# Kernel tuning notes

Hardware: AMD Instinct MI355X
Metric: run time of the kernel (lower is better)

## Reference

```python
import jax, jax.numpy as jnp
import numpy as np

D_MODEL = 1024
N_HEADS = 16
HIDDEN = int(D_MODEL * 4 * 2 / 3)  # 2730, matches torch int(d*4*2/3)
EPS = 1e-6


def setup_inputs() -> dict:
    key = jax.random.key(0)
    ks = jax.random.split(key, 8)
    B, T = 4, 2048
    s = 0.02
    return {
        "x": jax.random.normal(ks[0], (B, T, D_MODEL), dtype=jnp.float32),
        "w_attn": jax.random.normal(ks[1], (D_MODEL, 3 * D_MODEL), dtype=jnp.float32) * s,
        "w_proj": jax.random.normal(ks[2], (D_MODEL, D_MODEL), dtype=jnp.float32) * s,
        "w1": jax.random.normal(ks[3], (D_MODEL, HIDDEN), dtype=jnp.float32) * s,
        "w2": jax.random.normal(ks[4], (D_MODEL, HIDDEN), dtype=jnp.float32) * s,
        "w3": jax.random.normal(ks[5], (HIDDEN, D_MODEL), dtype=jnp.float32) * s,
        "g1": jnp.ones((D_MODEL,), dtype=jnp.float32),
        "g2": jnp.ones((D_MODEL,), dtype=jnp.float32),
    }


def rmsnorm(x, g):
    norm = jax.lax.rsqrt(jnp.mean(x * x, axis=-1, keepdims=True) + EPS)
    return x * norm * g


def reference(x, w_attn, w_proj, w1, w2, w3, g1, g2):
    B, T, C = x.shape
    H = N_HEADS
    hd = C // H

    # attention branch
    qkv = rmsnorm(x, g1) @ w_attn                     # [B,T,3C]
    q, k, v = jnp.split(qkv, 3, axis=-1)
    q = q.reshape(B, T, H, hd).transpose(0, 2, 1, 3)  # [B,H,T,hd]
    k = k.reshape(B, T, H, hd).transpose(0, 2, 1, 3)
    v = v.reshape(B, T, H, hd).transpose(0, 2, 1, 3)

    att = jnp.einsum("bhqd,bhkd->bhqk", q, k) / jnp.sqrt(jnp.float32(hd))
    causal = jnp.tril(jnp.ones((T, T), dtype=bool))
    att = jnp.where(causal[None, None], att, jnp.float32(-jnp.inf))
    att = jax.nn.softmax(att, axis=-1)
    y = jnp.einsum("bhqk,bhkd->bhqd", att, v)          # [B,H,T,hd]
    y = y.transpose(0, 2, 1, 3).reshape(B, T, C)
    attn_out = y @ w_proj

    # parallel MLP branch on ln_2(x) (note: applied to x, not x+attn)
    h = rmsnorm(x, g2)
    mlp_out = (jax.nn.silu(h @ w1) * (h @ w2)) @ w3

    # dropout is identity in eval mode
    return x + attn_out + mlp_out
```

## Files before the change

### kernel.cpp

```cpp
#include <hip/hip_runtime.h>

#define TT 2048
#define DM 1024
#define HPAD 2816
#define HID 2730

typedef __attribute__((ext_vector_type(4))) float f32x4;
typedef __attribute__((ext_vector_type(8))) short bf16x8;

static __device__ __forceinline__ float bf2f(short u) {
    union { float f; unsigned int i; } c; c.i = ((unsigned int)(unsigned short)u) << 16; return c.f;
}
static __device__ __forceinline__ short f2bf(float f) {
    union { float f; unsigned int i; } c; c.f = f;
    unsigned int i = c.i;
    unsigned int r = (i + 0x7fffu + ((i >> 16) & 1u)) >> 16;
    return (short)r;
}
static __device__ __forceinline__ unsigned int fbits(float f) {
    union { float f; unsigned int i; } c; c.f = f;
    return c.i;
}

static __device__ __forceinline__ void gload_lds16(const void* g, void* l) {
    __builtin_amdgcn_global_load_lds(
        (const __attribute__((address_space(1))) unsigned int*)g,
        (__attribute__((address_space(3))) unsigned int*)l, 16, 0, 0);
}

__global__ __launch_bounds__(256) void wprep(const float* __restrict__ in, short* __restrict__ out,
                                             int K, int N, int Kpad, int Npad) {
    __shared__ float tile[32][33];
    int kb = blockIdx.x * 32, nb = blockIdx.y * 32;
    int tx = threadIdx.x, ty = threadIdx.y;
    #pragma unroll
    for (int i = 0; i < 32; i += 8) {
        int k = kb + ty + i, n = nb + tx;
        float v = (k < K && n < N) ? in[(size_t)k * N + n] : 0.f;
        tile[tx][ty + i] = v;
    }
    __syncthreads();
    #pragma unroll
    for (int i = 0; i < 32; i += 8) {
        int n = nb + ty + i, k = kb + tx;
        if (n < Npad && k < Kpad) out[(size_t)n * Kpad + k] = f2bf(tile[ty + i][tx]);
    }
}

__global__ __launch_bounds__(256) void rmsnorm2(const float* __restrict__ x,
    const float* __restrict__ g1, const float* __restrict__ g2,
    short* __restrict__ xn1, short* __restrict__ xn2) {
    int row = blockIdx.x;
    const float* xr = x + (size_t)row * DM;
    int t = threadIdx.x;
    float4 v = ((const float4*)xr)[t];
    float ss = v.x*v.x + v.y*v.y + v.z*v.z + v.w*v.w;
    #pragma unroll
    for (int off = 1; off < 64; off <<= 1) ss += __shfl_xor(ss, off);
    __shared__ float red[4];
    if ((t & 63) == 0) red[t >> 6] = ss;
    __syncthreads();
    float tot = red[0] + red[1] + red[2] + red[3];
    float rs = rsqrtf(tot * (1.0f / DM) + 1e-6f);
    float4 G1 = ((const float4*)g1)[t];
    float4 G2 = ((const float4*)g2)[t];
    union { short s[4]; int2 v; } o1, o2;
    o1.s[0] = f2bf(v.x * rs * G1.x); o1.s[1] = f2bf(v.y * rs * G1.y);
    o1.s[2] = f2bf(v.z * rs * G1.z); o1.s[3] = f2bf(v.w * rs * G1.w);
    o2.s[0] = f2bf(v.x * rs * G2.x); o2.s[1] = f2bf(v.y * rs * G2.y);
    o2.s[2] = f2bf(v.z * rs * G2.z); o2.s[3] = f2bf(v.w * rs * G2.w);
    *(int2*)(xn1 + (size_t)row * DM + t * 4) = o1.v;
    *(int2*)(xn2 + (size_t)row * DM + t * 4) = o2.v;
}

template<int EPI>
__global__ __launch_bounds__(256) void gemm_bt(
    const short* __restrict__ A, const short* __restrict__ Bt,
    short* __restrict__ Cb, const float* __restrict__ X, float* __restrict__ Of,
    int M, int N, int K)
{
    __shared__ short As[128 * 64];
    __shared__ short Bs[128 * 64];
    int t = threadIdx.x;
    int wid = t >> 6, l = t & 63;
    int wm = wid >> 1, wn = wid & 1;

    int nwg = gridDim.x, bid = blockIdx.x;
    int wg = (bid & 7) * (nwg >> 3) + (bid >> 3);
    int tiles_n = N >> 7;
    int tm = wg / tiles_n, tn = wg % tiles_n;

    const short* Arow = A + (size_t)(tm * 128) * K;
    const short* Brow = Bt + (size_t)(tn * 128) * K;

    f32x4 acc[4][4];
    #pragma unroll
    for (int m = 0; m < 4; m++)
        #pragma unroll
        for (int n = 0; n < 4; n++) acc[m][n] = (f32x4){0.f, 0.f, 0.f, 0.f};

    for (int kt = 0; kt < K; kt += 64) {
        __syncthreads();
        #pragma unroll
        for (int i = 0; i < 4; i++) {
            int linear = i * 256 + t;
            int row = linear >> 3;
            int slot = linear & 7;
            int srcslot = slot ^ (row & 7);
            gload_lds16(Arow + (size_t)row * K + kt + srcslot * 8, (char*)As + linear * 16);
            gload_lds16(Brow + (size_t)row * K + kt + srcslot * 8, (char*)Bs + linear * 16);
        }
        __syncthreads();
        #pragma unroll
        for (int ks = 0; ks < 2; ks++) {
            bf16x8 af[4], bfr[4];
            #pragma unroll
            for (int m = 0; m < 4; m++) {
                int row = wm * 64 + m * 16 + (l & 15);
                af[m] = *(const bf16x8*)((char*)As + row * 128 + ((ks * 64 + (l >> 4) * 16) ^ ((row & 7) << 4)));
            }
            #pragma unroll
            for (int n = 0; n < 4; n++) {
                int row = wn * 64 + n * 16 + (l & 15);
                bfr[n] = *(const bf16x8*)((char*)Bs + row * 128 + ((ks * 64 + (l >> 4) * 16) ^ ((row & 7) << 4)));
            }
            #pragma unroll
            for (int m = 0; m < 4; m++)
                #pragma unroll
                for (int n = 0; n < 4; n++)
                    acc[m][n] = __builtin_amdgcn_mfma_f32_16x16x32_bf16(af[m], bfr[n], acc[m][n], 0, 0, 0);
        }
    }

    #pragma unroll
    for (int m = 0; m < 4; m++)
        #pragma unroll
        for (int n = 0; n < 4; n++)
            #pragma unroll
            for (int r = 0; r < 4; r++) {
                int row = tm * 128 + wm * 64 + m * 16 + (l >> 4) * 4 + r;
                int col = tn * 128 + wn * 64 + n * 16 + (l & 15);
                size_t idx = (size_t)row * N + col;
                float v = acc[m][n][r];
                if constexpr (EPI == 0) Cb[idx] = f2bf(v);
                else if constexpr (EPI == 1) Of[idx] = X[idx] + v;
                else if constexpr (EPI == 4) Of[idx] += v;
            }
}

__global__ __launch_bounds__(256) void gemm_fuse(
    const short* __restrict__ A1, const short* __restrict__ B1,
    const short* __restrict__ A2, const short* __restrict__ B2,
    const float* __restrict__ X, float* __restrict__ Of)
{
    __shared__ short As[128 * 64];
    __shared__ short Bs[128 * 64];
    int t = threadIdx.x;
    int wid = t >> 6, l = t & 63;
    int wm = wid >> 1, wn = wid & 1;

    int nwg = gridDim.x, bid = blockIdx.x;
    int wg = (bid & 7) * (nwg >> 3) + (bid >> 3);
    int tiles_n = 8;
    int tm = wg / tiles_n, tn = wg % tiles_n;

    f32x4 acc[4][4];
    #pragma unroll
    for (int m = 0; m < 4; m++)
        #pragma unroll
        for (int n = 0; n < 4; n++) acc[m][n] = (f32x4){0.f, 0.f, 0.f, 0.f};

    #pragma unroll 1
    for (int phase = 0; phase < 2; phase++) {
        const short* Arow = phase == 0 ? A1 + (size_t)(tm * 128) * 1024 : A2 + (size_t)(tm * 128) * HPAD;
        const short* Brow = phase == 0 ? B1 + (size_t)(tn * 128) * 1024 : B2 + (size_t)(tn * 128) * HPAD;
        int K = phase == 0 ? 1024 : HPAD;
        for (int kt = 0; kt < K; kt += 64) {
            __syncthreads();
            #pragma unroll
            for (int i = 0; i < 4; i++) {
                int linear = i * 256 + t;
                int row = linear >> 3;
                int slot = linear & 7;
                int srcslot = slot ^ (row & 7);
                gload_lds16(Arow + (size_t)row * K + kt + srcslot * 8, (char*)As + linear * 16);
                gload_lds16(Brow + (size_t)row * K + kt + srcslot * 8, (char*)Bs + linear * 16);
            }
            __syncthreads();
            #pragma unroll
            for (int ks = 0; ks < 2; ks++) {
                bf16x8 af[4], bfr[4];
                #pragma unroll
                for (int m = 0; m < 4; m++) {
                    int row = wm * 64 + m * 16 + (l & 15);
                    af[m] = *(const bf16x8*)((char*)As + row * 128 + ((ks * 64 + (l >> 4) * 16) ^ ((row & 7) << 4)));
                }
                #pragma unroll
                for (int n = 0; n < 4; n++) {
                    int row = wn * 64 + n * 16 + (l & 15);
                    bfr[n] = *(const bf16x8*)((char*)Bs + row * 128 + ((ks * 64 + (l >> 4) * 16) ^ ((row & 7) << 4)));
                }
                #pragma unroll
                for (int m = 0; m < 4; m++)
                    #pragma unroll
                    for (int n = 0; n < 4; n++)
                        acc[m][n] = __builtin_amdgcn_mfma_f32_16x16x32_bf16(af[m], bfr[n], acc[m][n], 0, 0, 0);
            }
        }
    }

    #pragma unroll
    for (int m = 0; m < 4; m++)
        #pragma unroll
        for (int n = 0; n < 4; n++)
            #pragma unroll
            for (int r = 0; r < 4; r++) {
                int row = tm * 128 + wm * 64 + m * 16 + (l >> 4) * 4 + r;
                int col = tn * 128 + wn * 64 + n * 16 + (l & 15);
                size_t idx = (size_t)row * 1024 + col;
                Of[idx] = X[idx] + acc[m][n][r];
            }
}

__global__ __launch_bounds__(512, 2) void gemm_mlp2(
    const short* __restrict__ A, const short* __restrict__ B1t, const short* __restrict__ B2t,
    short* __restrict__ Cb, int M, int N, int K)
{
    __shared__ short As[128 * 64];
    __shared__ short B1s[128 * 64];
    __shared__ short B2s[128 * 64];
    int t = threadIdx.x;
    int wid = t >> 6, l = t & 63;
    int wm = wid >> 2, wn = wid & 3;

    int nwg = gridDim.x, bid = blockIdx.x;
    int wg = (bid & 7) * (nwg >> 3) + (bid >> 3);
    int tiles_n = N >> 7;
    int tm = wg / tiles_n, tn = wg % tiles_n;

    const short* Arow  = A   + (size_t)(tm * 128) * K;
    const short* B1row = B1t + (size_t)(tn * 128) * K;
    const short* B2row = B2t + (size_t)(tn * 128) * K;

    f32x4 acc1[4][2], acc2[4][2];
    #pragma unroll
    for (int m = 0; m < 4; m++)
        #pragma unroll
        for (int n = 0; n < 2; n++) {
            acc1[m][n] = (f32x4){0.f, 0.f, 0.f, 0.f};
            acc2[m][n] = (f32x4){0.f, 0.f, 0.f, 0.f};
        }

    for (int kt = 0; kt < K; kt += 64) {
        __syncthreads();
        #pragma unroll
        for (int i = 0; i < 2; i++) {
            int linear = i * 512 + t;
            int row = linear >> 3;
            int slot = linear & 7;
            int srcslot = slot ^ (row & 7);
            gload_lds16(Arow  + (size_t)row * K + kt + srcslot * 8, (char*)As  + linear * 16);
            gload_lds16(B1row + (size_t)row * K + kt + srcslot * 8, (char*)B1s + linear * 16);
            gload_lds16(B2row + (size_t)row * K + kt + srcslot * 8, (char*)B2s + linear * 16);
        }
        __syncthreads();
        #pragma unroll
        for (int ks = 0; ks < 2; ks++) {
            bf16x8 af[4], b1[2], b2[2];
            #pragma unroll
            for (int m = 0; m < 4; m++) {
                int row = wm * 64 + m * 16 + (l & 15);
                int off = (ks * 64 + (l >> 4) * 16) ^ ((row & 7) << 4);
                af[m] = *(const bf16x8*)((char*)As + row * 128 + off);
            }
            #pragma unroll
            for (int n = 0; n < 2; n++) {
                int row = wn * 32 + n * 16 + (l & 15);
                int off = (ks * 64 + (l >> 4) * 16) ^ ((row & 7) << 4);
                b1[n] = *(const bf16x8*)((char*)B1s + row * 128 + off);
                b2[n] = *(const bf16x8*)((char*)B2s + row * 128 + off);
            }
            #pragma unroll
            for (int m = 0; m < 4; m++)
                #pragma unroll
                for (int n = 0; n < 2; n++) {
                    acc1[m][n] = __builtin_amdgcn_mfma_f32_16x16x32_bf16(af[m], b1[n], acc1[m][n], 0, 0, 0);
                    acc2[m][n] = __builtin_amdgcn_mfma_f32_16x16x32_bf16(af[m], b2[n], acc2[m][n], 0, 0, 0);
                }
        }
    }

    #pragma unroll
    for (int m = 0; m < 4; m++)
        #pragma unroll
        for (int n = 0; n < 2; n++)
            #pragma unroll
            for (int r = 0; r < 4; r++) {
                int row = tm * 128 + wm * 64 + m * 16 + (l >> 4) * 4 + r;
                int col = tn * 128 + wn * 32 + n * 16 + (l & 15);
                float v1 = acc1[m][n][r];
                float v2 = acc2[m][n][r];
                Cb[(size_t)row * N + col] = f2bf(v1 * (1.f / (1.f + __expf(-v1))) * v2);
            }
}

#define SM_C 0.18033688f
__global__ __launch_bounds__(512, 4) void attn(const short* __restrict__ qkv, short* __restrict__ y) {
    __shared__ short Ks[2][64 * 64];
    __shared__ short Vt[2][64 * 64];
    int bid = blockIdx.x;
    int xcd = bid & 7;
    int idx = bid >> 3;
    int bh  = xcd + 8 * (idx >> 3);
    int pair = idx & 7;
    int b = bh >> 4, h = bh & 15;
    int t = threadIdx.x, wid = t >> 6, l = t & 63;
    const size_t base = (size_t)b * TT * 3072;

    int krow = t >> 3, kslot = t & 7, ksrc = kslot ^ (krow & 7);
    int vrow = t >> 3, vch = t & 7;

    #pragma unroll
    for (int pass = 0; pass < 2; pass++) {
        int qt = pass == 0 ? (15 - pair) : pair;
        int q0 = qt * 128 + wid * 16;
        int qrow = q0 + (l & 15);

        bf16x8 qf[2];
        #pragma unroll
        for (int s = 0; s < 2; s++) {
            int row = q0 + (l & 15);
            bf16x8 q = *(const bf16x8*)(qkv + base + (size_t)row * 3072 + h * 64 + s * 32 + (l >> 4) * 8);
            #pragma unroll
            for (int i = 0; i < 8; i++) q[i] = f2bf(bf2f(q[i]) * SM_C);
            qf[s] = q;
        }

        f32x4 o[4];
        #pragma unroll
        for (int n = 0; n < 4; n++) o[n] = (f32x4){0.f, 0.f, 0.f, 0.f};
        float ll = 0.f;

        int nt = 2 * qt + 2;

        {
            gload_lds16(qkv + base + (size_t)krow * 3072 + 1024 + h * 64 + ksrc * 8,
                        (char*)Ks + t * 16);
            uint4 vv = *(const uint4*)(qkv + base + (size_t)vrow * 3072 + 2048 + h * 64 + vch * 8);
            const short* vs = (const short*)&vv;
            #pragma unroll
            for (int j = 0; j < 8; j++) {
                int d = vch * 8 + j;
                int byte = (d * 128 + vrow * 2) ^ (((j ^ vch) & 7) << 4);
                *(short*)((char*)Vt + byte) = vs[j];
            }
            __syncthreads();
        }

        int cur = 0;
        for (int it = 0; it < nt; ++it) {
            int kb = it << 6;
            bool have_next = (it + 1 < nt);
            uint4 vv;
            if (have_next) {
                int nkb = kb + 64;
                gload_lds16(qkv + base + (size_t)(nkb + krow) * 3072 + 1024 + h * 64 + ksrc * 8,
                            (char*)Ks + (cur ^ 1) * 8192 + t * 16);
                vv = *(const uint4*)(qkv + base + (size_t)(nkb + vrow) * 3072 + 2048 + h * 64 + vch * 8);
            }
            if (kb <= q0 + 15) {
                bool diag = (kb + 63 > q0);
                unsigned int pk[4][2];
                __builtin_amdgcn_s_setprio(1);
                #pragma unroll
                for (int j = 0; j < 4; j++) {
                    f32x4 z = (f32x4){0.f, 0.f, 0.f, 0.f};
                    #pragma unroll
                    for (int ks = 0; ks < 2; ks++) {
                        int row = j * 16 + (l & 15);
                        bf16x8 kf = *(const bf16x8*)((char*)Ks + cur * 8192 + row * 128 +
                                    ((ks * 64 + (l >> 4) * 16) ^ ((row & 7) << 4)));
                        z = __builtin_amdgcn_mfma_f32_16x16x32_bf16(kf, qf[ks], z, 0, 0, 0);
                    }
                    float p[4];
                    #pragma unroll
                    for (int r = 0; r < 4; r++) {
                        float v = z[r];
                        if (diag) {
                            int kcol = kb + j * 16 + (l >> 4) * 4 + r;
                            if (kcol > qrow) v = -3e38f;
                        }
                        p[r] = exp2f(v);
                        ll += p[r];
                    }
                    pk[j][0] = (fbits(p[1]) & 0xffff0000u) | (fbits(p[0]) >> 16);
                    pk[j][1] = (fbits(p[3]) & 0xffff0000u) | (fbits(p[2]) >> 16);
                }
                __builtin_amdgcn_s_setprio(0);

                #pragma unroll
                for (int ks = 0; ks < 2; ks++) {
                    union { unsigned int u[4]; bf16x8 v; } pa;
                    #pragma unroll
                    for (int w = 0; w < 4; w++) {
                        int src = (((l >> 4) & 1) << 5) | ((w >> 1) << 4) | (l & 15);
                        unsigned int a = __shfl(pk[2 * ks][w & 1], src);
                        unsigned int bb = __shfl(pk[2 * ks + 1][w & 1], src);
                        pa.u[w] = (l >> 5) ? bb : a;
                    }
                    __builtin_amdgcn_s_setprio(1);
                    #pragma unroll
                    for (int n = 0; n < 4; n++) {
                        int vr = n * 16 + (l & 15);
                        int f = (vr & 7) ^ ((vr >> 3) & 7);
                        bf16x8 vf = *(const bf16x8*)((char*)Vt + cur * 8192 + vr * 128 +
                                    ((ks * 64 + (l >> 4) * 16) ^ (f << 4)));
                        o[n] = __builtin_amdgcn_mfma_f32_16x16x32_bf16(pa.v, vf, o[n], 0, 0, 0);
                    }
                    __builtin_amdgcn_s_setprio(0);
                }
            }
            if (have_next) {
                const short* vs = (const short*)&vv;
                #pragma unroll
                for (int j = 0; j < 8; j++) {
                    int d = vch * 8 + j;
                    int byte = (d * 128 + vrow * 2) ^ (((j ^ vch) & 7) << 4);
                    *(short*)((char*)Vt + (cur ^ 1) * 8192 + byte) = vs[j];
                }
            }
            __syncthreads();
            cur ^= 1;
        }

        ll += __shfl_xor(ll, 16);
        ll += __shfl_xor(ll, 32);
        float inv = 1.f / ll;
        #pragma unroll
        for (int r = 0; r < 4; r++) {
            float invr = __shfl(inv, (l >> 4) * 4 + r);
            #pragma unroll
            for (int n = 0; n < 4; n++) {
                int row = q0 + (l >> 4) * 4 + r;
                int col = h * 64 + n * 16 + (l & 15);
                y[(size_t)(b * TT + row) * DM + col] = f2bf(o[n][r] * invr);
            }
        }
    }
}

extern "C" void kernel_launch(void* const* d_in, const int* in_sizes, int n_in,
                              void* d_out, int out_size, void* d_ws, size_t ws_size,
                              hipStream_t stream) {
    (void)in_sizes; (void)n_in; (void)out_size; (void)ws_size;
    const float* x      = (const float*)d_in[0];
    const float* w_attn = (const float*)d_in[1];
    const float* w_proj = (const float*)d_in[2];
    const float* w1     = (const float*)d_in[3];
    const float* w2     = (const float*)d_in[4];
    const float* w3     = (const float*)d_in[5];
    const float* g1     = (const float*)d_in[6];
    const float* g2     = (const float*)d_in[7];
    float* out = (float*)d_out;

    char* ws = (char*)d_ws;
    size_t off = 0;
    auto alloc = [&](size_t bytes) { char* p = ws + off; off += (bytes + 255) & ~(size_t)255; return p; };
    short* wattn_t = (short*)alloc((size_t)3072 * 1024 * 2);
    short* wproj_t = (short*)alloc((size_t)1024 * 1024 * 2);
    short* w1t     = (short*)alloc((size_t)HPAD * 1024 * 2);
    short* w2t     = (short*)alloc((size_t)HPAD * 1024 * 2);
    short* w3t     = (short*)alloc((size_t)1024 * HPAD * 2);
    short* xn1     = (short*)alloc((size_t)8192 * 1024 * 2);
    short* xn2     = (short*)alloc((size_t)8192 * 1024 * 2);
    short* qkvb    = (short*)alloc((size_t)8192 * 3072 * 2);
    short* yb      = (short*)alloc((size_t)8192 * 1024 * 2);
    short* hb      = (short*)alloc((size_t)8192 * HPAD * 2);

    dim3 tb(32, 8);
    wprep<<<dim3(32, 96), tb, 0, stream>>>(w_attn, wattn_t, 1024, 3072, 1024, 3072);
    wprep<<<dim3(32, 32), tb, 0, stream>>>(w_proj, wproj_t, 1024, 1024, 1024, 1024);
    wprep<<<dim3(32, 88), tb, 0, stream>>>(w1, w1t, 1024, HID, 1024, HPAD);
    wprep<<<dim3(32, 88), tb, 0, stream>>>(w2, w2t, 1024, HID, 1024, HPAD);
    wprep<<<dim3(88, 32), tb, 0, stream>>>(w3, w3t, HID, 1024, HPAD, 1024);

    rmsnorm2<<<8192, 256, 0, stream>>>(x, g1, g2, xn1, xn2);

    gemm_bt<0><<<1536, 256, 0, stream>>>(xn1, wattn_t, qkvb, nullptr, nullptr, 8192, 3072, 1024);
    attn<<<512, 512, 0, stream>>>(qkvb, yb);
    gemm_mlp2<<<1408, 512, 0, stream>>>(xn2, w1t, w2t, hb, 8192, HPAD, 1024);
    gemm_fuse<<<512, 256, 0, stream>>>(yb, wproj_t, hb, w3t, x, out);
}
```

Baseline: 342.8 us.

## Enlarge attention KV tile to 128 keys and pack V transpose stores

The attention kernel now processes 128 keys per iteration instead of 64. Each K/V LDS buffer doubles in size, occupancy drops to 2 blocks per CU, and the loop count halves, so there are fewer barriers per unit of work. V is transposed into LDS with packed 32-bit stores of two rows at a time using a new swizzle. The row-sum is split into four partial accumulators to shorten the dependency chain. In exchange, every warp now runs the full 128-key tile on the diagonal, including fully masked keys, and the lower occupancy could reduce latency hiding.

```diff
diff --git a/kernel.cpp b/kernel.cpp
--- a/kernel.cpp
+++ b/kernel.cpp
@@ -305,9 +305,9 @@
 }
 
 #define SM_C 0.18033688f
-__global__ __launch_bounds__(512, 4) void attn(const short* __restrict__ qkv, short* __restrict__ y) {
-    __shared__ short Ks[2][64 * 64];
-    __shared__ short Vt[2][64 * 64];
+__global__ __launch_bounds__(512, 2) void attn(const short* __restrict__ qkv, short* __restrict__ y) {
+    __shared__ short Ks[2][128 * 64];
+    __shared__ short Vt[2][64 * 128];
     int bid = blockIdx.x;
     int xcd = bid & 7;
     int idx = bid >> 3;
@@ -317,8 +317,7 @@
     int t = threadIdx.x, wid = t >> 6, l = t & 63;
     const size_t base = (size_t)b * TT * 3072;
 
-    int krow = t >> 3, kslot = t & 7, ksrc = kslot ^ (krow & 7);
-    int vrow = t >> 3, vch = t & 7;
+    int vrg = t >> 3, vch = t & 7;
 
     #pragma unroll
     for (int pass = 0; pass < 2; pass++) {
@@ -339,46 +338,61 @@
         f32x4 o[4];
         #pragma unroll
         for (int n = 0; n < 4; n++) o[n] = (f32x4){0.f, 0.f, 0.f, 0.f};
-        float ll = 0.f;
-
-        int nt = 2 * qt + 2;
+        float ll4[4];
+        #pragma unroll
+        for (int r = 0; r < 4; r++) ll4[r] = 0.f;
+
+        int nt = qt + 1;
 
         {
-            gload_lds16(qkv + base + (size_t)krow * 3072 + 1024 + h * 64 + ksrc * 8,
-                        (char*)Ks + t * 16);
-            uint4 vv = *(const uint4*)(qkv + base + (size_t)vrow * 3072 + 2048 + h * 64 + vch * 8);
-            const short* vs = (const short*)&vv;
+            #pragma unroll
+            for (int i = 0; i < 2; i++) {
+                int lin = i * 512 + t; int row = lin >> 3; int sl = lin & 7; int src = sl ^ (row & 7);
+                gload_lds16(qkv + base + (size_t)row * 3072 + 1024 + h * 64 + src * 8,
+                            (char*)Ks + lin * 16);
+            }
+            uint4 va = *(const uint4*)(qkv + base + (size_t)(vrg * 2)     * 3072 + 2048 + h * 64 + vch * 8);
+            uint4 vb = *(const uint4*)(qkv + base + (size_t)(vrg * 2 + 1) * 3072 + 2048 + h * 64 + vch * 8);
+            const short* s0 = (const short*)&va;
+            const short* s1 = (const short*)&vb;
             #pragma unroll
             for (int j = 0; j < 8; j++) {
                 int d = vch * 8 + j;
-                int byte = (d * 128 + vrow * 2) ^ (((j ^ vch) & 7) << 4);
-                *(short*)((char*)Vt + byte) = vs[j];
+                unsigned int pack = ((unsigned int)(unsigned short)s0[j]) |
+                                    (((unsigned int)(unsigned short)s1[j]) << 16);
+                int byte = (d * 256 + vrg * 4) ^ ((((d & 7) ^ (d >> 3)) & 7) << 4);
+                *(unsigned int*)((char*)Vt + byte) = pack;
             }
             __syncthreads();
         }
 
         int cur = 0;
         for (int it = 0; it < nt; ++it) {
-            int kb = it << 6;
+            int kb = it << 7;
             bool have_next = (it + 1 < nt);
-            uint4 vv;
+            uint4 va, vb;
             if (have_next) {
-                int nkb = kb + 64;
-                gload_lds16(qkv + base + (size_t)(nkb + krow) * 3072 + 1024 + h * 64 + ksrc * 8,
-                            (char*)Ks + (cur ^ 1) * 8192 + t * 16);
-                vv = *(const uint4*)(qkv + base + (size_t)(nkb + vrow) * 3072 + 2048 + h * 64 + vch * 8);
-            }
-            if (kb <= q0 + 15) {
-                bool diag = (kb + 63 > q0);
-                unsigned int pk[4][2];
+                int nkb = kb + 128;
+                #pragma unroll
+                for (int i = 0; i < 2; i++) {
+                    int lin = i * 512 + t; int row = lin >> 3; int sl = lin & 7; int src = sl ^ (row & 7);
+                    gload_lds16(qkv + base + (size_t)(nkb + row) * 3072 + 1024 + h * 64 + src * 8,
+                                (char*)Ks + (cur ^ 1) * 16384 + lin * 16);
+                }
+                va = *(const uint4*)(qkv + base + (size_t)(nkb + vrg * 2)     * 3072 + 2048 + h * 64 + vch * 8);
+                vb = *(const uint4*)(qkv + base + (size_t)(nkb + vrg * 2 + 1) * 3072 + 2048 + h * 64 + vch * 8);
+            }
+            {
+                bool diag = (it == qt);
+                unsigned int pk[8][2];
                 __builtin_amdgcn_s_setprio(1);
                 #pragma unroll
-                for (int j = 0; j < 4; j++) {
+                for (int j = 0; j < 8; j++) {
                     f32x4 z = (f32x4){0.f, 0.f, 0.f, 0.f};
                     #pragma unroll
                     for (int ks = 0; ks < 2; ks++) {
                         int row = j * 16 + (l & 15);
-                        bf16x8 kf = *(const bf16x8*)((char*)Ks + cur * 8192 + row * 128 +
+                        bf16x8 kf = *(const bf16x8*)((char*)Ks + cur * 16384 + row * 128 +
                                     ((ks * 64 + (l >> 4) * 16) ^ ((row & 7) << 4)));
                         z = __builtin_amdgcn_mfma_f32_16x16x32_bf16(kf, qf[ks], z, 0, 0, 0);
                     }
@@ -391,7 +405,7 @@
                             if (kcol > qrow) v = -3e38f;
                         }
                         p[r] = exp2f(v);
-                        ll += p[r];
+                        ll4[r] += p[r];
                     }
                     pk[j][0] = (fbits(p[1]) & 0xffff0000u) | (fbits(p[0]) >> 16);
                     pk[j][1] = (fbits(p[3]) & 0xffff0000u) | (fbits(p[2]) >> 16);
@@ -399,7 +413,7 @@
                 __builtin_amdgcn_s_setprio(0);
 
                 #pragma unroll
-                for (int ks = 0; ks < 2; ks++) {
+                for (int ks = 0; ks < 4; ks++) {
                     union { unsigned int u[4]; bf16x8 v; } pa;
                     #pragma unroll
                     for (int w = 0; w < 4; w++) {
@@ -413,7 +427,7 @@
                     for (int n = 0; n < 4; n++) {
                         int vr = n * 16 + (l & 15);
                         int f = (vr & 7) ^ ((vr >> 3) & 7);
-                        bf16x8 vf = *(const bf16x8*)((char*)Vt + cur * 8192 + vr * 128 +
+                        bf16x8 vf = *(const bf16x8*)((char*)Vt + cur * 16384 + vr * 256 +
                                     ((ks * 64 + (l >> 4) * 16) ^ (f << 4)));
                         o[n] = __builtin_amdgcn_mfma_f32_16x16x32_bf16(pa.v, vf, o[n], 0, 0, 0);
                     }
@@ -421,18 +435,22 @@
                 }
             }
             if (have_next) {
-                const short* vs = (const short*)&vv;
+                const short* s0 = (const short*)&va;
+                const short* s1 = (const short*)&vb;
                 #pragma unroll
                 for (int j = 0; j < 8; j++) {
                     int d = vch * 8 + j;
-                    int byte = (d * 128 + vrow * 2) ^ (((j ^ vch) & 7) << 4);
-                    *(short*)((char*)Vt + (cur ^ 1) * 8192 + byte) = vs[j];
+                    unsigned int pack = ((unsigned int)(unsigned short)s0[j]) |
+                                        (((unsigned int)(unsigned short)s1[j]) << 16);
+                    int byte = (d * 256 + vrg * 4) ^ ((((d & 7) ^ (d >> 3)) & 7) << 4);
+                    *(unsigned int*)((char*)Vt + (cur ^ 1) * 16384 + byte) = pack;
                 }
             }
             __syncthreads();
             cur ^= 1;
         }
 
+        float ll = (ll4[0] + ll4[1]) + (ll4[2] + ll4[3]);
         ll += __shfl_xor(ll, 16);
         ll += __shfl_xor(ll, 32);
         float inv = 1.f / ll;
```

Measured after the change: 361.9 us. 1.06x slower.

## Enlarge QKV GEMM tile to 256x128 and fold softmax scale into epilogue

Applied to the files above, without the earlier changes.

The QKV projection GEMM now uses 512-thread blocks with a 256x128 output tile, so each B tile loaded into shared memory is reused across twice as many rows and half as many workgroups run. MFMA sections are wrapped in s_setprio to favour the compute waves. The softmax scale is applied to the Q columns in the GEMM epilogue instead of rescaling Q inside the attention kernel. This adds LDS use per block and changes bf16 rounding order for Q slightly.

```diff
diff --git a/kernel.cpp b/kernel.cpp
--- a/kernel.cpp
+++ b/kernel.cpp
@@ -4,6 +4,7 @@
 #define DM 1024
 #define HPAD 2816
 #define HID 2730
+#define SM_C 0.18033688f
 
 typedef __attribute__((ext_vector_type(4))) float f32x4;
 typedef __attribute__((ext_vector_type(8))) short bf16x8;
@@ -74,12 +75,11 @@
 }
 
 template<int EPI>
-__global__ __launch_bounds__(256) void gemm_bt(
+__global__ __launch_bounds__(512, 4) void gemm256(
     const short* __restrict__ A, const short* __restrict__ Bt,
-    short* __restrict__ Cb, const float* __restrict__ X, float* __restrict__ Of,
-    int M, int N, int K)
+    short* __restrict__ Cb, int N, int K)
 {
-    __shared__ short As[128 * 64];
+    __shared__ short As[256 * 64];
     __shared__ short Bs[128 * 64];
     int t = threadIdx.x;
     int wid = t >> 6, l = t & 63;
@@ -90,25 +90,32 @@
     int tiles_n = N >> 7;
     int tm = wg / tiles_n, tn = wg % tiles_n;
 
-    const short* Arow = A + (size_t)(tm * 128) * K;
-    const short* Brow = Bt + (size_t)(tn * 128) * K;
-
     f32x4 acc[4][4];
     #pragma unroll
     for (int m = 0; m < 4; m++)
         #pragma unroll
         for (int n = 0; n < 4; n++) acc[m][n] = (f32x4){0.f, 0.f, 0.f, 0.f};
+
+    const short* Apan = A + (size_t)(tm * 256) * K;
+    const short* Bpan = Bt + (size_t)(tn * 128) * K;
 
     for (int kt = 0; kt < K; kt += 64) {
         __syncthreads();
         #pragma unroll
         for (int i = 0; i < 4; i++) {
-            int linear = i * 256 + t;
-            int row = linear >> 3;
-            int slot = linear & 7;
-            int srcslot = slot ^ (row & 7);
-            gload_lds16(Arow + (size_t)row * K + kt + srcslot * 8, (char*)As + linear * 16);
-            gload_lds16(Brow + (size_t)row * K + kt + srcslot * 8, (char*)Bs + linear * 16);
+            int lin = i * 512 + t;
+            int row = lin >> 3;
+            int slot = lin & 7;
+            int src = slot ^ (row & 7);
+            gload_lds16(Apan + (size_t)row * K + kt + src * 8, (char*)As + lin * 16);
+        }
+        #pragma unroll
+        for (int i = 0; i < 2; i++) {
+            int lin = i * 512 + t;
+            int row = lin >> 3;
+            int slot = lin & 7;
+            int src = slot ^ (row & 7);
+            gload_lds16(Bpan + (size_t)row * K + kt + src * 8, (char*)Bs + lin * 16);
         }
         __syncthreads();
         #pragma unroll
@@ -124,27 +131,29 @@
                 int row = wn * 64 + n * 16 + (l & 15);
                 bfr[n] = *(const bf16x8*)((char*)Bs + row * 128 + ((ks * 64 + (l >> 4) * 16) ^ ((row & 7) << 4)));
             }
+            __builtin_amdgcn_s_setprio(1);
             #pragma unroll
             for (int m = 0; m < 4; m++)
                 #pragma unroll
                 for (int n = 0; n < 4; n++)
                     acc[m][n] = __builtin_amdgcn_mfma_f32_16x16x32_bf16(af[m], bfr[n], acc[m][n], 0, 0, 0);
-        }
-    }
-
+            __builtin_amdgcn_s_setprio(0);
+        }
+    }
+
+    bool qcols = (EPI == 5) && (tn < 8);
     #pragma unroll
     for (int m = 0; m < 4; m++)
         #pragma unroll
         for (int n = 0; n < 4; n++)
             #pragma unroll
             for (int r = 0; r < 4; r++) {
-                int row = tm * 128 + wm * 64 + m * 16 + (l >> 4) * 4 + r;
+                int row = tm * 256 + wm * 64 + m * 16 + (l >> 4) * 4 + r;
                 int col = tn * 128 + wn * 64 + n * 16 + (l & 15);
                 size_t idx = (size_t)row * N + col;
                 float v = acc[m][n][r];
-                if constexpr (EPI == 0) Cb[idx] = f2bf(v);
-                else if constexpr (EPI == 1) Of[idx] = X[idx] + v;
-                else if constexpr (EPI == 4) Of[idx] += v;
+                if constexpr (EPI == 5) Cb[idx] = f2bf(qcols ? v * SM_C : v);
+                else Cb[idx] = f2bf(v);
             }
 }
 
@@ -304,7 +313,6 @@
             }
 }
 
-#define SM_C 0.18033688f
 __global__ __launch_bounds__(512, 4) void attn(const short* __restrict__ qkv, short* __restrict__ y) {
     __shared__ short Ks[2][64 * 64];
     __shared__ short Vt[2][64 * 64];
@@ -330,10 +338,7 @@
         #pragma unroll
         for (int s = 0; s < 2; s++) {
             int row = q0 + (l & 15);
-            bf16x8 q = *(const bf16x8*)(qkv + base + (size_t)row * 3072 + h * 64 + s * 32 + (l >> 4) * 8);
-            #pragma unroll
-            for (int i = 0; i < 8; i++) q[i] = f2bf(bf2f(q[i]) * SM_C);
-            qf[s] = q;
+            qf[s] = *(const bf16x8*)(qkv + base + (size_t)row * 3072 + h * 64 + s * 32 + (l >> 4) * 8);
         }
 
         f32x4 o[4];
@@ -486,7 +491,7 @@
 
     rmsnorm2<<<8192, 256, 0, stream>>>(x, g1, g2, xn1, xn2);
 
-    gemm_bt<0><<<1536, 256, 0, stream>>>(xn1, wattn_t, qkvb, nullptr, nullptr, 8192, 3072, 1024);
+    gemm256<5><<<768, 512, 0, stream>>>(xn1, wattn_t, qkvb, 3072, 1024);
     attn<<<512, 512, 0, stream>>>(qkvb, yb);
     gemm_mlp2<<<1408, 512, 0, stream>>>(xn2, w1t, w2t, hb, 8192, HPAD, 1024);
     gemm_fuse<<<512, 256, 0, stream>>>(yb, wproj_t, hb, w3t, x, out);
```

After: 341.5 us. About the same (-0.4%).
